# Kernel tuning notes

Measured on AMD Instinct MI355X. Metric: run time of the kernel, lower is better.

## Reference

```python
import jax, jax.numpy as jnp
import numpy as np

N, E, D, H, LAYERS = 50000, 800000, 128, 8, 2
LRELU_ALPHA = 0.2


def _seg_softmax(logits, seg, n):
    # numerically stable softmax over edges grouped by destination node
    m = jax.ops.segment_max(logits, seg, num_segments=n)
    z = jnp.exp(logits - m[seg])
    s = jax.ops.segment_sum(z, seg, num_segments=n)
    return z / jnp.maximum(s[seg], 1e-16)


def _gat_layer(x, src, dst, W, a_src, a_dst, concat):
    # W: [H, Fin, F'], a_src/a_dst: [H, F']
    n = x.shape[0]
    outs = []
    for h in range(W.shape[0]):  # loop over heads to bound peak memory
        Wh = x @ W[h]                              # [N, F']
        es = Wh @ a_src[h]                         # [N]
        ed = Wh @ a_dst[h]                         # [N]
        e = jax.nn.leaky_relu(es[src] + ed[dst], LRELU_ALPHA)  # [E]
        att = _seg_softmax(e, dst, n)              # [E]
        out = jax.ops.segment_sum(att[:, None] * Wh[src], dst, num_segments=n)
        outs.append(out)
    if concat:
        return jax.nn.elu(jnp.concatenate(outs, axis=-1))  # [N, H*F']
    return jnp.mean(jnp.stack(outs, axis=0), axis=0)        # [N, F']


def _rel_gcn_layer(x, src, dst, w, W):
    # weighted-adjacency GCN with row (in-degree) normalization + ReLU
    n = x.shape[0]
    deg = jax.ops.segment_sum(w, dst, num_segments=n)
    norm = w / jnp.maximum(deg[dst], 1e-16)        # [E]
    h = x @ W                                      # [N, Dout]
    agg = jax.ops.segment_sum(norm[:, None] * h[src], dst, num_segments=n)
    return jax.nn.relu(agg)


def setup_inputs() -> dict:
    key = jax.random.key(0)
    ks = jax.random.split(key, 12)
    s = 1.0 / np.sqrt(D)
    return {
        "x": jax.random.normal(ks[0], (N, D), dtype=jnp.float32),
        "edge_index": jax.random.randint(ks[1], (2, E), 0, N, dtype=jnp.int64),
        "edge_weight": jax.random.uniform(ks[2], (E,), dtype=jnp.float32),
        "gat_W0": jax.random.normal(ks[3], (H, D, D // H), dtype=jnp.float32) * s,
        "gat_a0_src": jax.random.normal(ks[4], (H, D // H), dtype=jnp.float32) * s,
        "gat_a0_dst": jax.random.normal(ks[5], (H, D // H), dtype=jnp.float32) * s,
        "gat_W1": jax.random.normal(ks[6], (H, D, D), dtype=jnp.float32) * s,
        "gat_a1_src": jax.random.normal(ks[7], (H, D), dtype=jnp.float32) * s,
        "gat_a1_dst": jax.random.normal(ks[8], (H, D), dtype=jnp.float32) * s,
        "gcn_W0": jax.random.normal(ks[9], (D, D), dtype=jnp.float32) * s,
        "gcn_W1": jax.random.normal(ks[10], (D, D), dtype=jnp.float32) * s,
    }


def reference(x, edge_index, edge_weight, gat_W0, gat_a0_src, gat_a0_dst,
              gat_W1, gat_a1_src, gat_a1_dst, gcn_W0, gcn_W1):
    src, dst = edge_index[0], edge_index[1]
    gat_params = [(gat_W0, gat_a0_src, gat_a0_dst), (gat_W1, gat_a1_src, gat_a1_dst)]
    gcn_params = [gcn_W0, gcn_W1]
    x1, x2 = x, x  # dropout is identity in eval mode
    for i in range(LAYERS):
        W, a_s, a_d = gat_params[i]
        x1 = _gat_layer(x1, src, dst, W, a_s, a_d, concat=(i != LAYERS - 1))
        x2 = _rel_gcn_layer(x2, src, dst, edge_weight, gcn_params[i])
    # cat along new last dim then MaxPool1d(2) == elementwise max of branches
    return jnp.maximum(x1, x2)
```

## Files before the change

kernel.cpp:

```cpp
#include <hip/hip_runtime.h>

#define LRELU_ALPHA 0.2f

typedef __attribute__((ext_vector_type(8))) short short8;
typedef __attribute__((ext_vector_type(4))) float float4v;
typedef __attribute__((ext_vector_type(2))) float f32x2;

__device__ __forceinline__ unsigned short f2bf(float f) {
  union { float f; unsigned u; } x; x.f = f;
  unsigned r = (x.u + 0x7fff + ((x.u >> 16) & 1)) >> 16;
  return (unsigned short)r;
}
__device__ __forceinline__ float bflo(unsigned u) {
  union { unsigned u; float f; } x; x.u = u << 16; return x.f;
}
__device__ __forceinline__ float bfhi(unsigned u) {
  union { unsigned u; float f; } x; x.u = u & 0xffff0000u; return x.f;
}
__device__ __forceinline__ f32x2 bfpair(unsigned u) {
  return (f32x2){bflo(u), bfhi(u)};
}
__device__ __forceinline__ unsigned packbf(float a, float b) {
  return (unsigned)f2bf(a) | ((unsigned)f2bf(b) << 16);
}


__global__ __launch_bounds__(256) void k_count(const int* __restrict__ dst,
                                               int* __restrict__ cnt, int E) {
  int e = blockIdx.x * 256 + threadIdx.x;
  if (e < E) atomicAdd(&cnt[dst[e]], 1);
}

__global__ __launch_bounds__(1024) void k_scan1(const int* __restrict__ cnt,
                                                int* __restrict__ lscan,
                                                int* __restrict__ bsum, int N) {
  __shared__ int sm[1024];
  int t = threadIdx.x;
  int base = blockIdx.x * 1024;
  int v = (base + t < N) ? cnt[base + t] : 0;
  sm[t] = v;
  __syncthreads();
  for (int off = 1; off < 1024; off <<= 1) {
    int x = (t >= off) ? sm[t - off] : 0;
    __syncthreads();
    sm[t] += x;
    __syncthreads();
  }
  if (base + t < N) lscan[base + t] = sm[t] - v;
  if (t == 1023) bsum[blockIdx.x] = sm[1023];
}

__global__ __launch_bounds__(64) void k_scan2(int* __restrict__ bsum,
                                              int* __restrict__ rowptrN, int nb) {
  int t = threadIdx.x;
  int v = (t < nb) ? bsum[t] : 0;
  int orig = v;
  for (int off = 1; off < 64; off <<= 1) {
    int y = __shfl_up(v, off, 64);
    if (t >= off) v += y;
  }
  if (t < nb) bsum[t] = v - orig;
  if (t == 63) *rowptrN = v;
}

__global__ __launch_bounds__(1024) void k_scan3(int* __restrict__ rowptr,
                                                int* __restrict__ cur,
                                                const int* __restrict__ bsum, int N) {
  int i = blockIdx.x * 1024 + threadIdx.x;
  if (i < N) {
    int v = rowptr[i] + bsum[blockIdx.x];
    rowptr[i] = v;
    cur[i] = v;
  }
}

__global__ __launch_bounds__(256) void k_scatter(const int* __restrict__ src,
                                                 const int* __restrict__ dst,
                                                 const float* __restrict__ w,
                                                 const float* __restrict__ logit0,
                                                 int* __restrict__ cur,
                                                 uint2* __restrict__ edata,
                                                 unsigned short* __restrict__ pedge,
                                                 int E) {
  int e = blockIdx.x * 256 + threadIdx.x;
  if (e >= E) return;
  int d = dst[e];
  int s = src[e];
  int p = atomicAdd(&cur[d], 1);
  edata[p] = make_uint2((unsigned)s, __float_as_uint(w[e]));
  float4 es0 = *(const float4*)(logit0 + (size_t)s * 16);
  float4 es1 = *(const float4*)(logit0 + (size_t)s * 16 + 4);
  float4 ed0 = *(const float4*)(logit0 + (size_t)d * 16 + 8);
  float4 ed1 = *(const float4*)(logit0 + (size_t)d * 16 + 12);
  float lg[8] = {es0.x + ed0.x, es0.y + ed0.y, es0.z + ed0.z, es0.w + ed0.w,
                 es1.x + ed1.x, es1.y + ed1.y, es1.z + ed1.z, es1.w + ed1.w};
  unsigned short o[8];
#pragma unroll
  for (int h = 0; h < 8; ++h) {
    float v = lg[h] > 0.f ? lg[h] : LRELU_ALPHA * lg[h];
    o[h] = f2bf(__expf(fminf(v, 80.f)));
  }
  ushort4 q0 = {o[0], o[1], o[2], o[3]};
  ushort4 q1 = {o[4], o[5], o[6], o[7]};
  *(ushort4*)(pedge + (size_t)p * 8) = q0;
  *(ushort4*)(pedge + (size_t)p * 8 + 4) = q1;
}

__global__ __launch_bounds__(256) void k_pack(const float* __restrict__ W0,
                                              const float* __restrict__ a0s,
                                              const float* __restrict__ a0d,
                                              const float* __restrict__ W1,
                                              const float* __restrict__ a1s,
                                              const float* __restrict__ a1d,
                                              const float* __restrict__ gw0,
                                              const float* __restrict__ gw1,
                                              unsigned short* __restrict__ W0catT,
                                              float* __restrict__ logitW,
                                              unsigned short* __restrict__ gw1T,
                                              unsigned short* __restrict__ va1T,
                                              unsigned short* __restrict__ WstackT) {
  int idx = blockIdx.x * 256 + threadIdx.x;
  if (idx < 32768) {
    int n = idx >> 7, k = idx & 127;
    int q = n >> 2, r = n & 3;
    float v;
    if (r < 2) {
      int o = 2 * q + r;
      int h = o >> 4, f = o & 15;
      v = W0[h * 2048 + k * 16 + f];
    } else {
      int j = 2 * q + (r - 2);
      v = gw0[k * 128 + j];
    }
    W0catT[idx] = f2bf(v);
  } else if (idx < 34816) {
    int j = idx - 32768;
    int k = j >> 4, c = j & 15;
    int h = (c < 8) ? c : c - 8;
    const float* a = (c < 8) ? a0s : a0d;
    float s = 0.f;
    for (int f = 0; f < 16; ++f) s += W0[h * 2048 + k * 16 + f] * a[h * 16 + f];
    logitW[j] = s;
  } else if (idx < 51200) {
    int j = idx - 34816;
    int n = j >> 7, k = j & 127;
    gw1T[j] = f2bf(gw1[k * 128 + n]);
  } else if (idx < 53248) {
    int j = idx - 51200;
    int c = j >> 7, k = j & 127;
    int h = c & 7;
    const float* a = (c < 8) ? a1s : a1d;
    float s = 0.f;
    for (int f = 0; f < 128; ++f) s += W1[h * 16384 + k * 128 + f] * a[h * 128 + f];
    va1T[j] = f2bf(s);
  } else if (idx < 184320) {
    int j = idx - 53248;
    int n = j >> 10, kk = j & 1023;
    int h = kk >> 7, k = kk & 127;
    WstackT[j] = f2bf(W1[h * 16384 + k * 128 + n] * 0.125f);
  }
}

__global__ __launch_bounds__(256) void k_prep(const float* __restrict__ x,
                                              const float* __restrict__ logitW,
                                              unsigned short* __restrict__ xb,
                                              float* __restrict__ logit0, int N) {
  __shared__ float sm[16][132];
  __shared__ float sw[2048];
  int t = threadIdx.x;
  int base = blockIdx.x * 16;
  int r = t >> 4, cc = (t & 15) * 8;
  const float* xr = x + (size_t)(base + r) * 128 + cc;
  float4 v0 = *(const float4*)xr;
  float4 v1 = *(const float4*)(xr + 4);
  ushort4 o0 = {f2bf(v0.x), f2bf(v0.y), f2bf(v0.z), f2bf(v0.w)};
  ushort4 o1 = {f2bf(v1.x), f2bf(v1.y), f2bf(v1.z), f2bf(v1.w)};
  *(ushort4*)(xb + (size_t)(base + r) * 128 + cc) = o0;
  *(ushort4*)(xb + (size_t)(base + r) * 128 + cc + 4) = o1;
  *(float4*)&sm[r][cc] = v0;
  *(float4*)&sm[r][cc + 4] = v1;
  *(float4*)&sw[t * 8] = *(const float4*)(logitW + t * 8);
  *(float4*)&sw[t * 8 + 4] = *(const float4*)(logitW + t * 8 + 4);
  __syncthreads();
  int c = t & 15;
  float acc = 0.f;
#pragma unroll
  for (int k = 0; k < 128; ++k) acc += sm[r][k] * sw[k * 16 + c];
  logit0[(size_t)(base + r) * 16 + c] = acc;
}

__global__ __launch_bounds__(256) void k_pedge(const float* __restrict__ logits,
                                               const uint2* __restrict__ edata,
                                               const int* __restrict__ rowptr,
                                               unsigned short* __restrict__ pedge,
                                               float* __restrict__ linv, int N) {
  int wave = threadIdx.x >> 6, lane = threadIdx.x & 63;
  int d = blockIdx.x * 4 + wave;
  if (d >= N) return;
  int j8 = lane >> 3, h = lane & 7;
  float edv = logits[(size_t)d * 16 + 8 + h];
  int beg = rowptr[d], end = rowptr[d + 1];
  float lsum = 0.f;
  for (int ii = beg + j8; ii < end; ii += 8) {
    unsigned s = edata[ii].x;
    float es = logits[(size_t)s * 16 + h];
    float lg = es + edv;
    lg = lg > 0.f ? lg : LRELU_ALPHA * lg;
    float p = __expf(fminf(lg, 80.f));
    lsum += p;
    pedge[(size_t)ii * 8 + h] = f2bf(p);
  }
  lsum += __shfl_xor(lsum, 8, 64);
  lsum += __shfl_xor(lsum, 16, 64);
  lsum += __shfl_xor(lsum, 32, 64);
  if (lane < 8) linv[(size_t)d * 8 + h] = lsum > 0.f ? 1.f / lsum : 0.f;
}

template <int NT, int OUT_BF16, int EPI>
__global__ __launch_bounds__(256) void k_mgemm(const unsigned short* __restrict__ A, int lda,
                                               const unsigned short* __restrict__ BT, int ldb,
                                               void* __restrict__ Cv, int ldc,
                                               const void* __restrict__ aux,
                                               int M, int Ncols, int K) {
  __shared__ unsigned short As[64][64];
  __shared__ unsigned short Bs[NT * 16][64];
  int tid = threadIdx.x;
  int w = tid >> 6, lane = tid & 63;
  int quad = lane >> 4, l16 = lane & 15;
  int row0 = blockIdx.x * 64;
  int c0 = blockIdx.y * (NT * 16);
  float4v acc[NT];
#pragma unroll
  for (int t = 0; t < NT; ++t) acc[t] = (float4v){0.f, 0.f, 0.f, 0.f};

  for (int k0 = 0; k0 < K; k0 += 64) {
    __syncthreads();
#pragma unroll
    for (int i = 0; i < 2; ++i) {
      int c = tid + i * 256;
      int r = c >> 3, kc = c & 7;
      uint4 v = {0u, 0u, 0u, 0u};
      int gr = row0 + r;
      if (gr < M) v = *(const uint4*)(A + (size_t)gr * lda + k0 + kc * 8);
      *(uint4*)(&As[r][(kc ^ (r & 7)) * 8]) = v;
    }
#pragma unroll
    for (int i = 0; i < (NT * 128 + 255) / 256; ++i) {
      int c = tid + i * 256;
      if (c < NT * 128) {
        int n = c >> 3, kc = c & 7;
        uint4 v = {0u, 0u, 0u, 0u};
        int gn = c0 + n;
        if (gn < Ncols) v = *(const uint4*)(BT + (size_t)gn * ldb + k0 + kc * 8);
        *(uint4*)(&Bs[n][(kc ^ (n & 7)) * 8]) = v;
      }
    }
    __syncthreads();
#pragma unroll
    for (int ks = 0; ks < 2; ++ks) {
      int m = w * 16 + l16;
      int ga = (ks * 4 + quad) ^ (m & 7);
      short8 a = *(const short8*)(&As[m][ga * 8]);
#pragma unroll
      for (int t = 0; t < NT; ++t) {
        int n = t * 16 + l16;
        int gb = (ks * 4 + quad) ^ (n & 7);
        short8 b = *(const short8*)(&Bs[n][gb * 8]);
        acc[t] = __builtin_amdgcn_mfma_f32_16x16x32_bf16(a, b, acc[t], 0, 0, 0);
      }
    }
  }
#pragma unroll
  for (int t = 0; t < NT; ++t) {
    int cc = c0 + t * 16 + l16;
    if (cc >= Ncols) continue;
#pragma unroll
    for (int i = 0; i < 4; ++i) {
      int rr = row0 + w * 16 + quad * 4 + i;
      if (rr >= M) continue;
      float v = acc[t][i];
      if (EPI == 1) {
        unsigned short us = ((const unsigned short*)aux)[(size_t)rr * ldc + cc];
        v = fmaxf(v, bflo((unsigned)us));
      }
      if (EPI == 2) {
        ((unsigned short*)Cv)[(size_t)rr * 256 + 4 * (cc >> 1) + 2 + (cc & 1)] = f2bf(v);
      } else if (OUT_BF16)
        ((unsigned short*)Cv)[(size_t)rr * ldc + cc] = f2bf(v);
      else
        ((float*)Cv)[(size_t)rr * ldc + cc] = v;
    }
  }
}

__global__ __launch_bounds__(256) void k_agg0(const unsigned short* __restrict__ feat0i,
                                              const int* __restrict__ rowptr,
                                              const uint2* __restrict__ edata,
                                              const unsigned short* __restrict__ pedge,
                                              unsigned short* __restrict__ x1c,
                                              unsigned short* __restrict__ x2,
                                              unsigned short* __restrict__ xh, int N) {
  __shared__ uint2 swl[4][64];
  __shared__ float pl[4][512];
  int wave = threadIdx.x >> 6, lane = threadIdx.x & 63;
  int d = blockIdx.x * 4 + wave;
  if (d >= N) return;
  int half = lane >> 5, lane2 = lane & 31;
  int head = lane2 >> 2;
  int beg = rowptr[d], end = rowptr[d + 1], deg = end - beg;
  f32x2 aa = {0.f, 0.f}, ab = {0.f, 0.f}, ga = {0.f, 0.f}, gb = {0.f, 0.f};
  float l = 0.f, wsum = 0.f;
  for (int base = 0; base < deg; base += 64) {
    int idx = beg + base + lane;
    uint2 sv = make_uint2(0u, 0u);
    uint4 q = make_uint4(0u, 0u, 0u, 0u);
    if (idx < end) {
      sv = edata[idx];
      q = *(const uint4*)(pedge + (size_t)idx * 8);
    }
    swl[wave][lane] = sv;
    float4 pa = make_float4(bflo(q.x), bfhi(q.x), bflo(q.y), bfhi(q.y));
    float4 pb = make_float4(bflo(q.z), bfhi(q.z), bflo(q.w), bfhi(q.w));
    *(float4*)&pl[wave][lane * 8] = pa;
    *(float4*)&pl[wave][lane * 8 + 4] = pb;
    int ng = deg - base; if (ng > 64) ng = 64;
    int tp = (ng + 1) >> 1;
    for (int t = 0; t < tp; ++t) {
      int e = 2 * t + half;
      uint2 sw = swl[wave][e];
      float p = pl[wave][e * 8 + head];
      float wj = __uint_as_float(sw.y);
      uint4 u = *(const uint4*)(feat0i + (size_t)sw.x * 256 + 8 * lane2);
      aa += bfpair(u.x) * p;
      ga += bfpair(u.y) * wj;
      ab += bfpair(u.z) * p;
      gb += bfpair(u.w) * wj;
      l += p;
      wsum += wj;
    }
  }
  aa.x += __shfl_xor(aa.x, 32, 64); aa.y += __shfl_xor(aa.y, 32, 64);
  ab.x += __shfl_xor(ab.x, 32, 64); ab.y += __shfl_xor(ab.y, 32, 64);
  ga.x += __shfl_xor(ga.x, 32, 64); ga.y += __shfl_xor(ga.y, 32, 64);
  gb.x += __shfl_xor(gb.x, 32, 64); gb.y += __shfl_xor(gb.y, 32, 64);
  l += __shfl_xor(l, 32, 64);
  wsum += __shfl_xor(wsum, 32, 64);
  if (half == 0) {
    float inv = l > 0.f ? 1.f / l : 0.f;
    float v0 = aa.x * inv, v1 = aa.y * inv, v2 = ab.x * inv, v3 = ab.y * inv;
    v0 = v0 > 0.f ? v0 : __expf(v0) - 1.f;
    v1 = v1 > 0.f ? v1 : __expf(v1) - 1.f;
    v2 = v2 > 0.f ? v2 : __expf(v2) - 1.f;
    v3 = v3 > 0.f ? v3 : __expf(v3) - 1.f;
    unsigned p0 = packbf(v0, v1), p1 = packbf(v2, v3);
    ((uint2*)x1c)[(size_t)d * 32 + lane2] = make_uint2(p0, p1);
    ((unsigned*)xh)[(size_t)d * 128 + 4 * lane2] = p0;
    ((unsigned*)xh)[(size_t)d * 128 + 4 * lane2 + 2] = p1;
    float ginv = 1.f / fmaxf(wsum, 1e-16f);
    float w0 = fmaxf(ga.x * ginv, 0.f), w1 = fmaxf(ga.y * ginv, 0.f);
    float w2 = fmaxf(gb.x * ginv, 0.f), w3 = fmaxf(gb.y * ginv, 0.f);
    ((uint2*)x2)[(size_t)d * 32 + lane2] = make_uint2(packbf(w0, w1), packbf(w2, w3));
  }
}

__global__ __launch_bounds__(256) void k_agg1(const unsigned short* __restrict__ xh,
                                              const int* __restrict__ rowptr,
                                              const uint2* __restrict__ edata,
                                              const unsigned short* __restrict__ pedge,
                                              const float* __restrict__ linv,
                                              unsigned short* __restrict__ aggbuf,
                                              unsigned short* __restrict__ x2f,
                                              int d0, int d1) {
  __shared__ uint2 swl[4][64];
  __shared__ float pl[4][512];
  int wave = threadIdx.x >> 6, lane = threadIdx.x & 63;
  int d = d0 + blockIdx.x * 4 + wave;
  if (d >= d1) return;
  int half = lane >> 5, lane2 = lane & 31;
  int beg = rowptr[d], end = rowptr[d + 1], deg = end - beg;
  f32x2 axA[8] = {}, axB[8] = {};
  f32x2 ga = {0.f, 0.f}, gb = {0.f, 0.f};
  float wsum = 0.f;
  for (int base = 0; base < deg; base += 64) {
    int idx = beg + base + lane;
    uint2 sv = make_uint2(0u, 0u);
    uint4 q = make_uint4(0u, 0u, 0u, 0u);
    if (idx < end) {
      sv = edata[idx];
      q = *(const uint4*)(pedge + (size_t)idx * 8);
    }
    swl[wave][lane] = sv;
    float4 pa = make_float4(bflo(q.x), bfhi(q.x), bflo(q.y), bfhi(q.y));
    float4 pb = make_float4(bflo(q.z), bfhi(q.z), bflo(q.w), bfhi(q.w));
    *(float4*)&pl[wave][lane * 8] = pa;
    *(float4*)&pl[wave][lane * 8 + 4] = pb;
    int ng = deg - base; if (ng > 64) ng = 64;
    int tp = (ng + 1) >> 1;
    for (int t = 0; t < tp; ++t) {
      int e = 2 * t + half;
      uint2 sw = swl[wave][e];
      float4 pv0 = *(const float4*)&pl[wave][e * 8];
      float4 pv1 = *(const float4*)&pl[wave][e * 8 + 4];
      float wj = __uint_as_float(sw.y);
      uint4 u = *(const uint4*)(xh + (size_t)sw.x * 256 + 8 * lane2);
      f32x2 xA = bfpair(u.x), hA = bfpair(u.y);
      f32x2 xB = bfpair(u.z), hB = bfpair(u.w);
      ga += hA * wj;
      gb += hB * wj;
      wsum += wj;
      axA[0] += xA * pv0.x; axB[0] += xB * pv0.x;
      axA[1] += xA * pv0.y; axB[1] += xB * pv0.y;
      axA[2] += xA * pv0.z; axB[2] += xB * pv0.z;
      axA[3] += xA * pv0.w; axB[3] += xB * pv0.w;
      axA[4] += xA * pv1.x; axB[4] += xB * pv1.x;
      axA[5] += xA * pv1.y; axB[5] += xB * pv1.y;
      axA[6] += xA * pv1.z; axB[6] += xB * pv1.z;
      axA[7] += xA * pv1.w; axB[7] += xB * pv1.w;
    }
  }
#pragma unroll
  for (int h = 0; h < 8; ++h) {
    axA[h].x += __shfl_xor(axA[h].x, 32, 64); axA[h].y += __shfl_xor(axA[h].y, 32, 64);
    axB[h].x += __shfl_xor(axB[h].x, 32, 64); axB[h].y += __shfl_xor(axB[h].y, 32, 64);
  }
  ga.x += __shfl_xor(ga.x, 32, 64); ga.y += __shfl_xor(ga.y, 32, 64);
  gb.x += __shfl_xor(gb.x, 32, 64); gb.y += __shfl_xor(gb.y, 32, 64);
  wsum += __shfl_xor(wsum, 32, 64);
  if (half == 0) {
    float4 i0 = *(const float4*)(linv + (size_t)d * 8);
    float4 i1 = *(const float4*)(linv + (size_t)d * 8 + 4);
    float invh[8] = {i0.x, i0.y, i0.z, i0.w, i1.x, i1.y, i1.z, i1.w};
    size_t lr2 = (size_t)(d - d0) * 256;
#pragma unroll
    for (int h = 0; h < 8; ++h) {
      ((uint2*)aggbuf)[lr2 + h * 32 + lane2] =
          make_uint2(packbf(axA[h].x * invh[h], axA[h].y * invh[h]),
                     packbf(axB[h].x * invh[h], axB[h].y * invh[h]));
    }
    float ginv = 1.f / fmaxf(wsum, 1e-16f);
    float w0 = fmaxf(ga.x * ginv, 0.f), w1 = fmaxf(ga.y * ginv, 0.f);
    float w2 = fmaxf(gb.x * ginv, 0.f), w3 = fmaxf(gb.y * ginv, 0.f);
    ((uint2*)x2f)[(size_t)d * 32 + lane2] = make_uint2(packbf(w0, w1), packbf(w2, w3));
  }
}


extern "C" void kernel_launch(void* const* d_in, const int* in_sizes, int n_in,
                              void* d_out, int out_size, void* d_ws, size_t ws_size,
                              hipStream_t stream) {
  const float* x   = (const float*)d_in[0];
  const int*   ei  = (const int*)d_in[1];
  const float* ew  = (const float*)d_in[2];
  const float* W0  = (const float*)d_in[3];
  const float* a0s = (const float*)d_in[4];
  const float* a0d = (const float*)d_in[5];
  const float* W1  = (const float*)d_in[6];
  const float* a1s = (const float*)d_in[7];
  const float* a1d = (const float*)d_in[8];
  const float* gw0 = (const float*)d_in[9];
  const float* gw1 = (const float*)d_in[10];
  float* out = (float*)d_out;

  const int N = in_sizes[0] / 128;
  const int E = in_sizes[1] / 2;
  const int* src = ei;
  const int* dst = ei + E;

  char* p = (char*)d_ws;
  auto carve = [&](size_t bytes) {
    void* r = (void*)p;
    p += (bytes + 255) & ~(size_t)255;
    return r;
  };
  int*   cnt    = (int*)carve((size_t)N * 4);
  int*   rowptr = (int*)carve((size_t)(N + 1) * 4);
  int*   cur    = (int*)carve((size_t)N * 4);
  int*   bsum   = (int*)carve(256 * 4);
  uint2* edata  = (uint2*)carve((size_t)E * 8);
  unsigned short* W0catT  = (unsigned short*)carve(32768 * 2);
  float*          logitW  = (float*)carve(2048 * 4);
  unsigned short* gw1T    = (unsigned short*)carve(16384 * 2);
  unsigned short* va1T    = (unsigned short*)carve(2048 * 2);
  unsigned short* WstackT = (unsigned short*)carve(131072 * 2);
  unsigned short* x1c  = (unsigned short*)carve((size_t)N * 128 * 2);
  unsigned short* x2   = (unsigned short*)carve((size_t)N * 128 * 2);
  unsigned short* x2f  = (unsigned short*)carve((size_t)N * 128 * 2);
  float*          esed = (float*)carve((size_t)N * 16 * 4);
  unsigned short* xh   = (unsigned short*)carve((size_t)N * 256 * 2);
  unsigned short* pedge = (unsigned short*)carve((size_t)E * 8 * 2);
  float*          linv1 = (float*)carve((size_t)N * 8 * 4);
  const int CH = 25600;
  size_t ph1 = ((size_t)N * 128 * 2 + 255) & ~(size_t)255;
  size_t ph2 = ph1 + (((size_t)N * 256 * 2 + 255) & ~(size_t)255);
  size_t ph3 = ph2 + (((size_t)N * 16 * 4 + 255) & ~(size_t)255);
  size_t scratch_sz = (size_t)CH * 1024 * 2;
  if (ph3 > scratch_sz) scratch_sz = ph3;
  char* scratch = (char*)carve(scratch_sz);
  unsigned short* xb     = (unsigned short*)scratch;
  unsigned short* feat0i = (unsigned short*)(scratch + ph1);
  float*          logit0 = (float*)(scratch + ph2);
  unsigned short* aggbuf = (unsigned short*)scratch;

  int gE = (E + 255) / 256;
  int nb = (N + 1023) / 1024;
  int gM = (N + 63) / 64;
  int gD = (N + 3) / 4;

  hipMemsetAsync(cnt, 0, (size_t)N * 4, stream);
  k_count<<<gE, 256, 0, stream>>>(dst, cnt, E);
  k_scan1<<<nb, 1024, 0, stream>>>(cnt, rowptr, bsum, N);
  k_scan2<<<1, 64, 0, stream>>>(bsum, rowptr + N, nb);
  k_scan3<<<nb, 1024, 0, stream>>>(rowptr, cur, bsum, N);

  k_pack<<<(184320 + 255) / 256, 256, 0, stream>>>(W0, a0s, a0d, W1, a1s, a1d, gw0,
                                                   gw1, W0catT, logitW, gw1T, va1T,
                                                   WstackT);
  k_prep<<<(N + 15) / 16, 256, 0, stream>>>(x, logitW, xb, logit0, N);

  k_scatter<<<gE, 256, 0, stream>>>(src, dst, ew, logit0, cur, edata, pedge, E);

  k_mgemm<8, 1, 0><<<dim3(gM, 2), 256, 0, stream>>>(xb, 128, W0catT, 128, feat0i, 256,
                                                    nullptr, N, 256, 128);
  k_agg0<<<gD, 256, 0, stream>>>(feat0i, rowptr, edata, pedge, x1c, x2, xh, N);

  k_mgemm<1, 0, 0><<<dim3(gM, 1), 256, 0, stream>>>(x1c, 128, va1T, 128, esed, 16,
                                                    nullptr, N, 16, 128);
  k_mgemm<8, 1, 2><<<dim3(gM, 1), 256, 0, stream>>>(x2, 128, gw1T, 128, xh, 256,
                                                    nullptr, N, 128, 128);

  k_pedge<<<gD, 256, 0, stream>>>(esed, edata, rowptr, pedge, linv1, N);

  for (int d0 = 0; d0 < N; d0 += CH) {
    int d1 = d0 + CH < N ? d0 + CH : N;
    int chN = d1 - d0;
    k_agg1<<<(chN + 3) / 4, 256, 0, stream>>>(xh, rowptr, edata, pedge, linv1,
                                              aggbuf, x2f, d0, d1);
    k_mgemm<8, 0, 1><<<dim3((chN + 63) / 64, 1), 256, 0, stream>>>(
        aggbuf, 1024, WstackT, 1024, out + (size_t)d0 * 128, 128,
        x2f + (size_t)d0 * 128, chN, 128, 1024);
  }
}
```

Before: 492.3 us.

## Store layer-0 projected features in FP8 and unroll the gather-aggregate loop

The first GEMM now writes its 256-wide per-node feature rows as FP8 bytes instead of bf16. The layer-0 aggregation kernel gathers 8 bytes per lane instead of 16 and decodes them with the packed fp8-to-f32 conversion builtins. The edge loop is also unrolled by two so two gathers are in flight at once. This halves gather traffic for the first aggregation, which is bandwidth bound, at the cost of FP8 precision on intermediate features and a possible accuracy-tolerance risk.

```diff
diff --git a/kernel.cpp b/kernel.cpp
--- a/kernel.cpp
+++ b/kernel.cpp
@@ -285,6 +285,9 @@
       }
       if (EPI == 2) {
         ((unsigned short*)Cv)[(size_t)rr * 256 + 4 * (cc >> 1) + 2 + (cc & 1)] = f2bf(v);
+      } else if (EPI == 3) {
+        int enc = __builtin_amdgcn_cvt_pk_fp8_f32(v, v, 0, false);
+        ((unsigned char*)Cv)[(size_t)rr * ldc + cc] = (unsigned char)(enc & 0xff);
       } else if (OUT_BF16)
         ((unsigned short*)Cv)[(size_t)rr * ldc + cc] = f2bf(v);
       else
@@ -293,7 +296,7 @@
   }
 }
 
-__global__ __launch_bounds__(256) void k_agg0(const unsigned short* __restrict__ feat0i,
+__global__ __launch_bounds__(256) void k_agg0(const unsigned char* __restrict__ feat8,
                                               const int* __restrict__ rowptr,
                                               const uint2* __restrict__ edata,
                                               const unsigned short* __restrict__ pedge,
@@ -325,18 +328,39 @@
     *(float4*)&pl[wave][lane * 8 + 4] = pb;
     int ng = deg - base; if (ng > 64) ng = 64;
     int tp = (ng + 1) >> 1;
-    for (int t = 0; t < tp; ++t) {
+    int t = 0;
+    for (; t + 2 <= tp; t += 2) {
+      int e0 = 2 * t + half, e1 = e0 + 2;
+      uint2 sw0 = swl[wave][e0], sw1 = swl[wave][e1];
+      float p0 = pl[wave][e0 * 8 + head], p1 = pl[wave][e1 * 8 + head];
+      uint2 u0 = *(const uint2*)(feat8 + (size_t)sw0.x * 256 + 8 * lane2);
+      uint2 u1 = *(const uint2*)(feat8 + (size_t)sw1.x * 256 + 8 * lane2);
+      float w0 = __uint_as_float(sw0.y), w1 = __uint_as_float(sw1.y);
+      f32x2 gA0 = __builtin_amdgcn_cvt_pk_f32_fp8(u0.x, false);
+      f32x2 cA0 = __builtin_amdgcn_cvt_pk_f32_fp8(u0.x, true);
+      f32x2 gB0 = __builtin_amdgcn_cvt_pk_f32_fp8(u0.y, false);
+      f32x2 cB0 = __builtin_amdgcn_cvt_pk_f32_fp8(u0.y, true);
+      aa += gA0 * p0; ga += cA0 * w0; ab += gB0 * p0; gb += cB0 * w0;
+      l += p0; wsum += w0;
+      f32x2 gA1 = __builtin_amdgcn_cvt_pk_f32_fp8(u1.x, false);
+      f32x2 cA1 = __builtin_amdgcn_cvt_pk_f32_fp8(u1.x, true);
+      f32x2 gB1 = __builtin_amdgcn_cvt_pk_f32_fp8(u1.y, false);
+      f32x2 cB1 = __builtin_amdgcn_cvt_pk_f32_fp8(u1.y, true);
+      aa += gA1 * p1; ga += cA1 * w1; ab += gB1 * p1; gb += cB1 * w1;
+      l += p1; wsum += w1;
+    }
+    for (; t < tp; ++t) {
       int e = 2 * t + half;
       uint2 sw = swl[wave][e];
       float p = pl[wave][e * 8 + head];
       float wj = __uint_as_float(sw.y);
-      uint4 u = *(const uint4*)(feat0i + (size_t)sw.x * 256 + 8 * lane2);
-      aa += bfpair(u.x) * p;
-      ga += bfpair(u.y) * wj;
-      ab += bfpair(u.z) * p;
-      gb += bfpair(u.w) * wj;
-      l += p;
-      wsum += wj;
+      uint2 u = *(const uint2*)(feat8 + (size_t)sw.x * 256 + 8 * lane2);
+      f32x2 gA = __builtin_amdgcn_cvt_pk_f32_fp8(u.x, false);
+      f32x2 cA = __builtin_amdgcn_cvt_pk_f32_fp8(u.x, true);
+      f32x2 gB = __builtin_amdgcn_cvt_pk_f32_fp8(u.y, false);
+      f32x2 cB = __builtin_amdgcn_cvt_pk_f32_fp8(u.y, true);
+      aa += gA * p; ga += cA * wj; ab += gB * p; gb += cB * wj;
+      l += p; wsum += wj;
     }
   }
   aa.x += __shfl_xor(aa.x, 32, 64); aa.y += __shfl_xor(aa.y, 32, 64);
@@ -491,13 +515,13 @@
   float*          linv1 = (float*)carve((size_t)N * 8 * 4);
   const int CH = 25600;
   size_t ph1 = ((size_t)N * 128 * 2 + 255) & ~(size_t)255;
-  size_t ph2 = ph1 + (((size_t)N * 256 * 2 + 255) & ~(size_t)255);
+  size_t ph2 = ph1 + (((size_t)N * 256 + 255) & ~(size_t)255);
   size_t ph3 = ph2 + (((size_t)N * 16 * 4 + 255) & ~(size_t)255);
   size_t scratch_sz = (size_t)CH * 1024 * 2;
   if (ph3 > scratch_sz) scratch_sz = ph3;
   char* scratch = (char*)carve(scratch_sz);
   unsigned short* xb     = (unsigned short*)scratch;
-  unsigned short* feat0i = (unsigned short*)(scratch + ph1);
+  unsigned char*  feat8  = (unsigned char*)(scratch + ph1);
   float*          logit0 = (float*)(scratch + ph2);
   unsigned short* aggbuf = (unsigned short*)scratch;
 
@@ -519,9 +543,9 @@
 
   k_scatter<<<gE, 256, 0, stream>>>(src, dst, ew, logit0, cur, edata, pedge, E);
 
-  k_mgemm<8, 1, 0><<<dim3(gM, 2), 256, 0, stream>>>(xb, 128, W0catT, 128, feat0i, 256,
+  k_mgemm<8, 1, 3><<<dim3(gM, 2), 256, 0, stream>>>(xb, 128, W0catT, 128, feat8, 256,
                                                     nullptr, N, 256, 128);
-  k_agg0<<<gD, 256, 0, stream>>>(feat0i, rowptr, edata, pedge, x1c, x2, xh, N);
+  k_agg0<<<gD, 256, 0, stream>>>(feat8, rowptr, edata, pedge, x1c, x2, xh, N);
 
   k_mgemm<1, 0, 0><<<dim3(gM, 1), 256, 0, stream>>>(x1c, 128, va1T, 128, esed, 16,
                                                     nullptr, N, 16, 128);
```

New measurement: 464.1 us. 5.7% less time.
